# Performance work log

Hardware: AMD Instinct MI355X
Metric: run time of the kernel (lower is better)

## Reference

```python
import jax, jax.numpy as jnp
import numpy as np

CONF_THRES = 0.25
IOU_THRES = 0.45
MAX_DET = 1000
MAX_WH = 4096.0  # class offset used by YOLOv5 for class-aware NMS
K = 1024         # fixed candidate count (static-shape stand-in for conf filtering)


def xywh2xyxy(b):
    cx, cy, w, h = b[..., 0], b[..., 1], b[..., 2], b[..., 3]
    return jnp.stack([cx - w / 2, cy - h / 2, cx + w / 2, cy + h / 2], axis=-1)


def pairwise_iou(boxes):
    # boxes: [K,4] xyxy -> [K,K] IoU
    x1, y1, x2, y2 = boxes[:, 0], boxes[:, 1], boxes[:, 2], boxes[:, 3]
    area = (x2 - x1) * (y2 - y1)
    ix1 = jnp.maximum(x1[:, None], x1[None, :])
    iy1 = jnp.maximum(y1[:, None], y1[None, :])
    ix2 = jnp.minimum(x2[:, None], x2[None, :])
    iy2 = jnp.minimum(y2[:, None], y2[None, :])
    inter = jnp.clip(ix2 - ix1, 0.0) * jnp.clip(iy2 - iy1, 0.0)
    return inter / (area[:, None] + area[None, :] - inter + 1e-9)


def nms_image(pred):
    # pred: [N, 5+nc] = xywh, obj, class scores
    boxes = xywh2xyxy(pred[:, :4])                 # [N,4]
    scores = pred[:, 5:] * pred[:, 4:5]            # conf = obj * cls
    conf = jnp.max(scores, axis=-1)                # [N]
    cls = jnp.argmax(scores, axis=-1)              # [N] int
    masked = jnp.where(conf > CONF_THRES, conf, -1.0)
    top_conf, idx = jax.lax.top_k(masked, K)       # sorted desc
    cand_boxes = boxes[idx]                        # [K,4]
    cand_cls = cls[idx]                            # [K]
    cand_valid = top_conf > 0.0                    # below-threshold slots are -1
    # class-aware NMS: offset boxes per class so different classes never overlap
    off_boxes = cand_boxes + (cand_cls.astype(pred.dtype) * MAX_WH)[:, None]
    iou = pairwise_iou(off_boxes)                  # [K,K]

    def step(suppressed, i):
        keep_i = jnp.logical_and(jnp.logical_not(suppressed[i]), cand_valid[i])
        suppressed = jnp.where(keep_i, jnp.logical_or(suppressed, iou[i] > IOU_THRES), suppressed)
        return suppressed, keep_i

    _, keep = jax.lax.scan(step, jnp.zeros((K,), dtype=bool), jnp.arange(K))
    sel_score = jnp.where(keep, top_conf, -1.0)
    fin_score, fin_idx = jax.lax.top_k(sel_score, MAX_DET)
    ok = fin_score > 0.0
    det = jnp.concatenate(
        [cand_boxes[fin_idx],
         top_conf[fin_idx][:, None],
         cand_cls[fin_idx].astype(pred.dtype)[:, None]],
        axis=-1,
    )  # [MAX_DET, 6] = x1,y1,x2,y2,conf,cls
    return jnp.where(ok[:, None], det, 0.0)


def setup_inputs() -> dict:
    key = jax.random.key(0)
    k1, k2, k3, k4 = jax.random.split(key, 4)
    B, N, NC = 16, 25200, 80
    cxcy = jax.random.uniform(k1, (B, N, 2), dtype=jnp.float32) * 640.0
    wh = jax.random.uniform(k2, (B, N, 2), dtype=jnp.float32) * 96.0 + 4.0
    obj = jax.random.uniform(k3, (B, N, 1), dtype=jnp.float32)
    cls = jax.random.uniform(k4, (B, N, NC), dtype=jnp.float32)
    pred = jnp.concatenate([cxcy, wh, obj, cls], axis=-1)
    return {"pred": pred}


def reference(pred):
    # [B, MAX_DET, 6] zero-padded detections per image
    return jax.vmap(nms_image)(pred)
```

## Files before the change

kernel.cpp:

```cpp
#include <hip/hip_runtime.h>
#include <stdint.h>

typedef unsigned int u32;
typedef unsigned long long u64;

#define BB 16
#define NN 25200
#define ROWLEN 85
#define KCAND 1024
#define MAXDET 1000
#define CONF_T 0.25f
#define IOU_T 0.45f
#define MAX_WH 4096.0f
#define KBASE 0xBE800000u

__device__ __forceinline__ u32 f2key(float f) {
  u32 u = __float_as_uint(f);
  return (u & 0x80000000u) ? ~u : (u | 0x80000000u);
}
__device__ __forceinline__ float key2f(u32 k) {
  u32 u = (k & 0x80000000u) ? (k & 0x7FFFFFFFu) : ~k;
  return __uint_as_float(u);
}

__global__ __launch_bounds__(64) void k_score(const float* __restrict__ pred,
                                              float* __restrict__ masked,
                                              int* __restrict__ clsArr) {
  __shared__ float sh[64 * ROWLEN];
  const int t = threadIdx.x;
  const size_t blk = (size_t)blockIdx.x;
  const float4* src = (const float4*)(pred + blk * (64 * ROWLEN));
  float4* dst = (float4*)sh;
  #pragma unroll
  for (int i = 0; i < 21; ++i) dst[t + 64 * i] = src[t + 64 * i];
  if (t < 16) dst[t + 64 * 21] = src[t + 64 * 21];
  __syncthreads();
  const float* row = sh + t * ROWLEN;
  float obj = row[4];
  float v0 = -INFINITY, v1 = -INFINITY, v2 = -INFINITY, v3 = -INFINITY;
  int j0 = 0, j1 = 20, j2 = 40, j3 = 60;
  #pragma unroll
  for (int c = 0; c < 20; ++c) {
    float s0 = obj * row[5 + c];
    float s1 = obj * row[25 + c];
    float s2 = obj * row[45 + c];
    float s3 = obj * row[65 + c];
    if (s0 > v0) { v0 = s0; j0 = c; }
    if (s1 > v1) { v1 = s1; j1 = 20 + c; }
    if (s2 > v2) { v2 = s2; j2 = 40 + c; }
    if (s3 > v3) { v3 = s3; j3 = 60 + c; }
  }
  float v = v0; int j = j0;
  if (v1 > v) { v = v1; j = j1; }
  if (v2 > v) { v = v2; j = j2; }
  if (v3 > v) { v = v3; j = j3; }
  size_t r = blk * 64 + t;
  masked[r] = (v > CONF_T) ? v : -1.0f;
  clsArr[r] = j;
}

__device__ __forceinline__ void bt_apply(u64& e, u64 p, int m, int j, int k) {
  bool lower = ((m & j) == 0);
  bool dir = ((m & k) == 0);
  bool takeMax = (lower == dir);
  u64 mx = e > p ? e : p;
  u64 mn = e > p ? p : e;
  e = takeMax ? mx : mn;
}

__global__ __launch_bounds__(1024, 4) void k_select(const float* __restrict__ pred,
                                                    const float* __restrict__ masked,
                                                    const int* __restrict__ clsArr,
                                                    float* __restrict__ candScore,
                                                    float* __restrict__ candBox,
                                                    int* __restrict__ candCls) {
  __shared__ u32 hist[16][257];
  __shared__ u64 buf[2048];
  __shared__ u32 sh_sel, sh_rem, sh_cnt;
  const int b = blockIdx.x;
  const int tid = threadIdx.x;
  const int lane = tid & 63;
  const int wv = tid >> 6;
  const float* m = masked + (size_t)b * NN;
  u32* histflat = (u32*)hist;

  u32 rr[25];
  #pragma unroll
  for (int it = 0; it < 25; ++it) {
    int n0 = tid + it * 1024;
    float val = (n0 < NN) ? m[n0] : -1.0f;
    u32 r = f2key(val) - KBASE;
    rr[it] = (val > 0.0f) ? r : 0u;
  }

  u32 prefix = 0, himask = 0, remaining = KCAND;
  #pragma unroll
  for (int pass = 0; pass < 3; ++pass) {
    int shift = 16 - 8 * pass;
    for (int i = tid; i < 16 * 257; i += 1024) histflat[i] = 0;
    __syncthreads();
    #pragma unroll
    for (int it = 0; it < 25; ++it) {
      u32 r = rr[it];
      if (r != 0u && (r & himask) == prefix)
        atomicAdd(&hist[wv][(r >> shift) & 255], 1u);
    }
    __syncthreads();
    if (wv == 0) {
      u32 c0 = 0, c1 = 0, c2 = 0, c3 = 0;
      #pragma unroll
      for (int w = 0; w < 16; ++w) {
        c0 += hist[w][4 * lane + 0];
        c1 += hist[w][4 * lane + 1];
        c2 += hist[w][4 * lane + 2];
        c3 += hist[w][4 * lane + 3];
      }
      u32 tl = c0 + c1 + c2 + c3;
      u32 incl = tl;
      #pragma unroll
      for (int off = 1; off <= 32; off <<= 1) {
        u32 o = __shfl_down(incl, off, 64);
        if (lane + off < 64) incl += o;
      }
      u32 S0 = incl;
      u32 S1 = S0 - c0;
      u32 S2 = S1 - c1;
      u32 S3 = S2 - c2;
      u32 S4 = S3 - c3;
      u32 rem = remaining;
      if (S0 >= rem && S1 < rem) { sh_sel = 4 * lane + 0; sh_rem = rem - S1; }
      if (S1 >= rem && S2 < rem) { sh_sel = 4 * lane + 1; sh_rem = rem - S2; }
      if (S2 >= rem && S3 < rem) { sh_sel = 4 * lane + 2; sh_rem = rem - S3; }
      if (S3 >= rem && S4 < rem) { sh_sel = 4 * lane + 3; sh_rem = rem - S4; }
    }
    __syncthreads();
    prefix |= (sh_sel << shift);
    remaining = sh_rem;
    himask |= (0xFFu << shift);
    __syncthreads();
  }
  const u32 T = prefix;
  if (tid == 0) sh_cnt = 0;
  __syncthreads();
  #pragma unroll
  for (int it = 0; it < 25; ++it) {
    int n0 = tid + it * 1024;
    u32 r = rr[it];
    bool match = (r >= T);
    u64 bal = __ballot(match);
    if (bal) {
      int leader = __ffsll((unsigned long long)bal) - 1;
      u32 base = 0;
      u32 cnt = (u32)__popcll(bal);
      if (lane == leader) base = atomicAdd(&sh_cnt, cnt);
      base = __shfl(base, leader, 64);
      if (match) {
        u32 pos = base + (u32)__popcll(bal & ((1ull << lane) - 1ull));
        if (pos < 2048) buf[pos] = ((u64)r << 32) | (u32)(~(u32)n0);
      }
    }
  }
  __syncthreads();
  u32 c = sh_cnt; if (c > 2048) c = 2048;
  for (int t = tid; t < 2048; t += 1024) if (t >= (int)c) buf[t] = 0;
  __syncthreads();

  u64 e0 = buf[tid];
  u64 e1 = buf[tid + 1024];
  #pragma unroll
  for (int k = 2; k <= 64; k <<= 1) {
    #pragma unroll
    for (int j = k >> 1; j > 0; j >>= 1) {
      u64 p0 = __shfl_xor(e0, j, 64);
      u64 p1 = __shfl_xor(e1, j, 64);
      bt_apply(e0, p0, tid, j, k);
      bt_apply(e1, p1, tid + 1024, j, k);
    }
  }
  for (int k = 128; k <= 2048; k <<= 1) {
    int jstart = k >> 1;
    if (k == 2048) {
      u64 mx = e0 > e1 ? e0 : e1;
      u64 mn = e0 > e1 ? e1 : e0;
      e0 = mx; e1 = mn;
      jstart = 512;
    }
    for (int j = jstart; j >= 64; j >>= 1) {
      buf[tid] = e0; buf[tid + 1024] = e1;
      __syncthreads();
      u64 p0 = buf[tid ^ j];
      u64 p1 = buf[(tid ^ j) + 1024];
      bt_apply(e0, p0, tid, j, k);
      bt_apply(e1, p1, tid + 1024, j, k);
      __syncthreads();
    }
    #pragma unroll
    for (int j = 32; j > 0; j >>= 1) {
      u64 p0 = __shfl_xor(e0, j, 64);
      u64 p1 = __shfl_xor(e1, j, 64);
      bt_apply(e0, p0, tid, j, k);
      bt_apply(e1, p1, tid + 1024, j, k);
    }
  }
  {
    u64 e = e0;
    u32 r = (u32)(e >> 32);
    u32 idx = ~(u32)e;
    if (idx >= NN) idx = 0;
    float sc = key2f(r + KBASE);
    size_t g = (size_t)b * KCAND + tid;
    candScore[g] = sc;
    const float* p = pred + ((size_t)b * NN + idx) * ROWLEN;
    float cx = p[0], cy = p[1], w = p[2], h = p[3];
    float4 bx;
    bx.x = cx - 0.5f * w;
    bx.y = cy - 0.5f * h;
    bx.z = cx + 0.5f * w;
    bx.w = cy + 0.5f * h;
    ((float4*)candBox)[g] = bx;
    candCls[g] = clsArr[(size_t)b * NN + idx];
  }
}

__global__ __launch_bounds__(256) void k_iou(const float* __restrict__ candBox,
                                             const int* __restrict__ candCls,
                                             u64* __restrict__ matT) {
  #pragma clang fp contract(off)
  __shared__ float sx1[KCAND], sy1[KCAND], sx2[KCAND], sy2[KCAND], sar[KCAND];
  const int b = blockIdx.y;
  const int r0 = blockIdx.x * 64;
  const int tid = threadIdx.x;
  for (int i = tid; i < KCAND; i += 256) {
    float4 bx = ((const float4*)candBox)[(size_t)b * KCAND + i];
    float off = (float)candCls[(size_t)b * KCAND + i] * MAX_WH;
    float x1 = bx.x + off, y1 = bx.y + off, x2 = bx.z + off, y2 = bx.w + off;
    sx1[i] = x1; sy1[i] = y1; sx2[i] = x2; sy2[i] = y2;
    sar[i] = (x2 - x1) * (y2 - y1);
  }
  __syncthreads();
  const int row = r0 + (tid & 63);
  const int wbase = tid >> 6;
  float rx1 = sx1[row], ry1 = sy1[row], rx2 = sx2[row], ry2 = sy2[row], rar = sar[row];
  for (int q = 0; q < 4; ++q) {
    int w = wbase + q * 4;
    int jb = w << 6;
    u64 mk = 0;
    for (int kk = 0; kk < 64; ++kk) {
      int jj = jb + kk;
      float ix1 = fmaxf(rx1, sx1[jj]);
      float iy1 = fmaxf(ry1, sy1[jj]);
      float ix2 = fminf(rx2, sx2[jj]);
      float iy2 = fminf(ry2, sy2[jj]);
      float dx = fmaxf(ix2 - ix1, 0.0f);
      float dy = fmaxf(iy2 - iy1, 0.0f);
      float inter = dx * dy;
      float den = rar + sar[jj];
      den = den - inter;
      den = den + 1e-9f;
      float iou = inter / den;
      if (iou > IOU_T) mk |= (1ull << kk);
    }
    matT[(((size_t)b * 16 + w) << 10) + row] = mk;
  }
}

#define TRIDX(c, cp) (((c) * ((c)-1)) / 2 + (cp))
__global__ __launch_bounds__(256, 1) void k_scan_out(const u64* __restrict__ matT,
                                                     const float* __restrict__ candScore,
                                                     const float* __restrict__ candBox,
                                                     const int* __restrict__ candCls,
                                                     float* __restrict__ out) {
  __shared__ u64 sKeep[16];
  const int b = blockIdx.x;
  const int tid = threadIdx.x;
  const u64* Mb = matT + ((size_t)b << 14);

  if (tid < 64) {
    const int lane = tid;
    u64 vw[16], dg[16], tri[120], kcw[16];
    #pragma unroll
    for (int w = 0; w < 16; ++w) {
      float sc = candScore[(size_t)b * KCAND + w * 64 + lane];
      vw[w] = __ballot(sc > 0.0f);
    }
    #pragma unroll
    for (int c = 0; c < 16; ++c)
      dg[c] = Mb[((size_t)c << 10) + c * 64 + lane];
    #pragma unroll
    for (int c = 1; c < 16; ++c) {
      #pragma unroll
      for (int cp = 0; cp < c; ++cp)
        tri[TRIDX(c, cp)] = Mb[((size_t)c << 10) + cp * 64 + lane];
    }

    #pragma unroll
    for (int c = 0; c < 16; ++c) {
      u64 acc = 0;
      #pragma unroll
      for (int cp = 0; cp < 15; ++cp) {
        if (cp < c) {
          if ((kcw[cp] >> lane) & 1ull) acc |= tri[TRIDX(c, cp)];
        }
      }
      #pragma unroll
      for (int st = 1; st < 64; st <<= 1) acc |= __shfl_xor(acc, st, 64);
      u64 d = dg[c];
      u64 s = acc;
      u64 kc = 0;
      u64 vc = vw[c];
      #pragma unroll
      for (int g = 0; g < 8; ++g) {
        u64 dgp[8];
        #pragma unroll
        for (int j = 0; j < 8; ++j) dgp[j] = __shfl(d, g * 8 + j, 64);
        #pragma unroll
        for (int j = 0; j < 8; ++j) {
          int i = g * 8 + j;
          bool ok = !((s >> i) & 1ull) && ((vc >> i) & 1ull);
          if (ok) { s |= dgp[j]; kc |= (1ull << i); }
        }
      }
      kcw[c] = kc;
    }
    if (lane < 16) sKeep[lane] = kcw[lane];
  }
  __syncthreads();

  int total = 0;
  #pragma unroll
  for (int w = 0; w < 16; ++w) total += __popcll(sKeep[w]);
  int kept_eff = total < MAXDET ? total : MAXDET;
  float* outb = out + (size_t)b * MAXDET * 6;
  #pragma unroll
  for (int rr2 = 0; rr2 < 4; ++rr2) {
    const int t = tid + rr2 * 256;
    u64 word = sKeep[t >> 6];
    int bit = (int)((word >> (t & 63)) & 1ull);
    int rank = 0;
    for (int w = 0; w < (t >> 6); ++w) rank += __popcll(sKeep[w]);
    rank += __popcll(word & ((1ull << (t & 63)) - 1ull));
    if (bit && rank < MAXDET) {
      size_t g = (size_t)b * KCAND + t;
      float4 bx = ((const float4*)candBox)[g];
      float sc = candScore[g];
      float cf = (float)candCls[g];
      float* o = outb + (size_t)rank * 6;
      o[0] = bx.x; o[1] = bx.y; o[2] = bx.z; o[3] = bx.w; o[4] = sc; o[5] = cf;
    }
    if (t < MAXDET && t >= kept_eff) {
      float* o = outb + (size_t)t * 6;
      o[0] = 0.f; o[1] = 0.f; o[2] = 0.f; o[3] = 0.f; o[4] = 0.f; o[5] = 0.f;
    }
  }
}

extern "C" void kernel_launch(void* const* d_in, const int* in_sizes, int n_in,
                              void* d_out, int out_size, void* d_ws, size_t ws_size,
                              hipStream_t stream) {
  const float* pred = (const float*)d_in[0];
  float* out = (float*)d_out;
  char* ws = (char*)d_ws;
  size_t o = 0;
  float* masked    = (float*)(ws + o); o += (size_t)BB * NN * 4;
  int*   clsArr    = (int*)  (ws + o); o += (size_t)BB * NN * 4;
  float* candScore = (float*)(ws + o); o += (size_t)BB * KCAND * 4;
  float* candBox   = (float*)(ws + o); o += (size_t)BB * KCAND * 16;
  int*   candCls   = (int*)  (ws + o); o += (size_t)BB * KCAND * 4;
  o = (o + 255) & ~(size_t)255;
  u64*   matT      = (u64*)  (ws + o); o += (size_t)BB * KCAND * 16 * 8;

  const int rows = BB * NN;
  k_score<<<rows / 64, 64, 0, stream>>>(pred, masked, clsArr);
  k_select<<<BB, 1024, 0, stream>>>(pred, masked, clsArr, candScore, candBox, candCls);
  k_iou<<<dim3(16, BB), 256, 0, stream>>>(candBox, candCls, matT);
  k_scan_out<<<BB, 256, 0, stream>>>(matT, candScore, candBox, candCls, out);
}
```

Before: 309.0 us.

## Build global score histogram in scoring kernel to replace per-image radix passes

The scoring kernel now atomically adds each valid score into a per-image 65536-bin global histogram keyed by the upper bits of the order-preserving key. A new zero kernel clears that histogram before scoring. The select kernel then finds the top-1024 threshold bin with a two-level suffix scan over that histogram, replacing three serial shared-memory radix passes that only 16 blocks ran. The cost is an extra launch, global atomics in the wide scoring kernel, and a coarser threshold that may admit more candidates into the sort buffer.

```diff
diff --git a/kernel.cpp b/kernel.cpp
--- a/kernel.cpp
+++ b/kernel.cpp
@@ -13,6 +13,7 @@
 #define IOU_T 0.45f
 #define MAX_WH 4096.0f
 #define KBASE 0xBE800000u
+#define NHBIN 65536
 
 __device__ __forceinline__ u32 f2key(float f) {
   u32 u = __float_as_uint(f);
@@ -23,9 +24,14 @@
   return __uint_as_float(u);
 }
 
+__global__ __launch_bounds__(1024) void k_zero(uint4* __restrict__ histv) {
+  histv[(size_t)blockIdx.x * 1024 + threadIdx.x] = make_uint4(0, 0, 0, 0);
+}
+
 __global__ __launch_bounds__(64) void k_score(const float* __restrict__ pred,
                                               float* __restrict__ masked,
-                                              int* __restrict__ clsArr) {
+                                              int* __restrict__ clsArr,
+                                              u32* __restrict__ hist) {
   __shared__ float sh[64 * ROWLEN];
   const int t = threadIdx.x;
   const size_t blk = (size_t)blockIdx.x;
@@ -55,8 +61,14 @@
   if (v2 > v) { v = v2; j = j2; }
   if (v3 > v) { v = v3; j = j3; }
   size_t r = blk * 64 + t;
-  masked[r] = (v > CONF_T) ? v : -1.0f;
+  bool valid = (v > CONF_T);
+  masked[r] = valid ? v : -1.0f;
   clsArr[r] = j;
+  if (valid) {
+    u32 b = (u32)(r / NN);
+    u32 rk = f2key(v) - KBASE;
+    atomicAdd(&hist[(size_t)b * NHBIN + (rk >> 8)], 1u);
+  }
 }
 
 __device__ __forceinline__ void bt_apply(u64& e, u64 p, int m, int j, int k) {
@@ -71,98 +83,85 @@
 __global__ __launch_bounds__(1024, 4) void k_select(const float* __restrict__ pred,
                                                     const float* __restrict__ masked,
                                                     const int* __restrict__ clsArr,
+                                                    const u32* __restrict__ hist,
                                                     float* __restrict__ candScore,
                                                     float* __restrict__ candBox,
                                                     int* __restrict__ candCls) {
-  __shared__ u32 hist[16][257];
   __shared__ u64 buf[2048];
-  __shared__ u32 sh_sel, sh_rem, sh_cnt;
+  __shared__ u32 waveTot[16];
+  __shared__ u32 sh_base, sh_snext, sh_T, sh_cnt;
   const int b = blockIdx.x;
   const int tid = threadIdx.x;
   const int lane = tid & 63;
   const int wv = tid >> 6;
+  const u32* hb = hist + (size_t)b * NHBIN;
   const float* m = masked + (size_t)b * NN;
-  u32* histflat = (u32*)hist;
-
-  u32 rr[25];
+
+  float vals[25];
   #pragma unroll
   for (int it = 0; it < 25; ++it) {
     int n0 = tid + it * 1024;
-    float val = (n0 < NN) ? m[n0] : -1.0f;
-    u32 r = f2key(val) - KBASE;
-    rr[it] = (val > 0.0f) ? r : 0u;
-  }
-
-  u32 prefix = 0, himask = 0, remaining = KCAND;
-  #pragma unroll
-  for (int pass = 0; pass < 3; ++pass) {
-    int shift = 16 - 8 * pass;
-    for (int i = tid; i < 16 * 257; i += 1024) histflat[i] = 0;
-    __syncthreads();
-    #pragma unroll
-    for (int it = 0; it < 25; ++it) {
-      u32 r = rr[it];
-      if (r != 0u && (r & himask) == prefix)
-        atomicAdd(&hist[wv][(r >> shift) & 255], 1u);
-    }
-    __syncthreads();
-    if (wv == 0) {
-      u32 c0 = 0, c1 = 0, c2 = 0, c3 = 0;
-      #pragma unroll
-      for (int w = 0; w < 16; ++w) {
-        c0 += hist[w][4 * lane + 0];
-        c1 += hist[w][4 * lane + 1];
-        c2 += hist[w][4 * lane + 2];
-        c3 += hist[w][4 * lane + 3];
-      }
-      u32 tl = c0 + c1 + c2 + c3;
-      u32 incl = tl;
-      #pragma unroll
-      for (int off = 1; off <= 32; off <<= 1) {
-        u32 o = __shfl_down(incl, off, 64);
-        if (lane + off < 64) incl += o;
-      }
-      u32 S0 = incl;
-      u32 S1 = S0 - c0;
-      u32 S2 = S1 - c1;
-      u32 S3 = S2 - c2;
-      u32 S4 = S3 - c3;
-      u32 rem = remaining;
-      if (S0 >= rem && S1 < rem) { sh_sel = 4 * lane + 0; sh_rem = rem - S1; }
-      if (S1 >= rem && S2 < rem) { sh_sel = 4 * lane + 1; sh_rem = rem - S2; }
-      if (S2 >= rem && S3 < rem) { sh_sel = 4 * lane + 2; sh_rem = rem - S3; }
-      if (S3 >= rem && S4 < rem) { sh_sel = 4 * lane + 3; sh_rem = rem - S4; }
-    }
-    __syncthreads();
-    prefix |= (sh_sel << shift);
-    remaining = sh_rem;
-    himask |= (0xFFu << shift);
-    __syncthreads();
-  }
-  const u32 T = prefix;
+    vals[it] = (n0 < NN) ? m[n0] : -1.0f;
+  }
+
+  u32 sloc = 0;
+  const int base = tid * 64;
+  for (int i = 0; i < 64; ++i) sloc += hb[base + i];
+  u32 incl = sloc;
+  #pragma unroll
+  for (int off = 1; off <= 32; off <<= 1) {
+    u32 o = __shfl_down(incl, off, 64);
+    if (lane + off < 64) incl += o;
+  }
+  if (lane == 0) waveTot[wv] = incl;
+  __syncthreads();
+  u32 wsuf = 0;
+  for (int w = wv + 1; w < 16; ++w) wsuf += waveTot[w];
+  u32 S_t = incl + wsuf;
+  u32 S_n = S_t - sloc;
+  if (S_t >= KCAND && S_n < KCAND) { sh_base = (u32)base; sh_snext = S_n; }
   if (tid == 0) sh_cnt = 0;
   __syncthreads();
+  if (wv == 0) {
+    u32 bv = hb[sh_base + lane];
+    u32 suf = bv;
+    #pragma unroll
+    for (int off = 1; off <= 32; off <<= 1) {
+      u32 o = __shfl_down(suf, off, 64);
+      if (lane + off < 64) suf += o;
+    }
+    u32 Sl = suf + sh_snext;
+    u32 Snl = Sl - bv;
+    if (Sl >= KCAND && Snl < KCAND) {
+      u32 tt = (sh_base + lane) << 8;
+      sh_T = tt ? tt : 1u;
+    }
+  }
+  __syncthreads();
+  const u32 T = sh_T;
+
   #pragma unroll
   for (int it = 0; it < 25; ++it) {
     int n0 = tid + it * 1024;
-    u32 r = rr[it];
+    float val = vals[it];
+    u32 r = (val > 0.0f) ? (f2key(val) - KBASE) : 0u;
     bool match = (r >= T);
     u64 bal = __ballot(match);
     if (bal) {
       int leader = __ffsll((unsigned long long)bal) - 1;
-      u32 base = 0;
+      u32 bpos = 0;
       u32 cnt = (u32)__popcll(bal);
-      if (lane == leader) base = atomicAdd(&sh_cnt, cnt);
-      base = __shfl(base, leader, 64);
+      if (lane == leader) bpos = atomicAdd(&sh_cnt, cnt);
+      bpos = __shfl(bpos, leader, 64);
       if (match) {
-        u32 pos = base + (u32)__popcll(bal & ((1ull << lane) - 1ull));
+        u32 pos = bpos + (u32)__popcll(bal & ((1ull << lane) - 1ull));
         if (pos < 2048) buf[pos] = ((u64)r << 32) | (u32)(~(u32)n0);
       }
     }
   }
   __syncthreads();
   u32 c = sh_cnt; if (c > 2048) c = 2048;
-  for (int t = tid; t < 2048; t += 1024) if (t >= (int)c) buf[t] = 0;
+  for (int t2 = tid; t2 < 2048; t2 += 1024) if (t2 >= (int)c) buf[t2] = 0;
   __syncthreads();
 
   u64 e0 = buf[tid];
@@ -368,10 +367,12 @@
   int*   candCls   = (int*)  (ws + o); o += (size_t)BB * KCAND * 4;
   o = (o + 255) & ~(size_t)255;
   u64*   matT      = (u64*)  (ws + o); o += (size_t)BB * KCAND * 16 * 8;
+  u32*   hist      = (u32*)  (ws + o); o += (size_t)BB * NHBIN * 4;
 
   const int rows = BB * NN;
-  k_score<<<rows / 64, 64, 0, stream>>>(pred, masked, clsArr);
-  k_select<<<BB, 1024, 0, stream>>>(pred, masked, clsArr, candScore, candBox, candCls);
+  k_zero<<<256, 1024, 0, stream>>>((uint4*)hist);
+  k_score<<<rows / 64, 64, 0, stream>>>(pred, masked, clsArr, hist);
+  k_select<<<BB, 1024, 0, stream>>>(pred, masked, clsArr, hist, candScore, candBox, candCls);
   k_iou<<<dim3(16, BB), 256, 0, stream>>>(candBox, candCls, matT);
   k_scan_out<<<BB, 256, 0, stream>>>(matT, candScore, candBox, candCls, out);
 }
```

Result: no change. 314.0 us (+1.6%).
